# Kernel tuning notes

Measured on AMD Instinct MI355X. Metric: run time of the kernel, lower is better.

## Reference

```python
import jax, jax.numpy as jnp
import numpy as np

CHEB_K = 3


def setup_inputs() -> dict:
    key = jax.random.key(0)
    k1, k2, k3 = jax.random.split(key, 3)
    B, N, C = 64, 2048, 64
    E, O = 16, 64
    x = jax.random.normal(k1, (B, N, C), dtype=jnp.float32)
    node_embeddings = jax.random.normal(k2, (N, E), dtype=jnp.float32)
    # xavier-uniform-like init for weights_pool (embed_dim, cheb_k, dim_in, dim_out)
    fan_in, fan_out = E * CHEB_K * C, O
    limit = float(np.sqrt(6.0 / (fan_in + fan_out)))
    weights_pool = jax.random.uniform(k3, (E, CHEB_K, C, O), dtype=jnp.float32,
                                      minval=-limit, maxval=limit)
    bias_pool = jnp.zeros((E, O), dtype=jnp.float32)
    return {"x": x, "node_embeddings": node_embeddings,
            "weights_pool": weights_pool, "bias_pool": bias_pool}


def reference(x, node_embeddings, weights_pool, bias_pool):
    N = node_embeddings.shape[0]
    # adaptive adjacency: softmax(relu(E E^T)) row-wise   [N, N]
    supports = jax.nn.softmax(jax.nn.relu(node_embeddings @ node_embeddings.T), axis=1)
    # Chebyshev recurrence: T0 = I, T1 = A, Tk = 2*A*T_{k-1} - T_{k-2}
    support_set = [jnp.eye(N, dtype=supports.dtype), supports]
    for _ in range(2, CHEB_K):
        support_set.append(2.0 * supports @ support_set[-1] - support_set[-2])
    supports_k = jnp.stack(support_set, axis=0)  # [K, N, N]
    # per-node dynamic weights / bias from pools
    weights = jnp.einsum('nd,dkio->nkio', node_embeddings, weights_pool)  # [N,K,C,O]
    bias = node_embeddings @ bias_pool                                    # [N,O]
    # graph conv: gather Chebyshev features then per-node grouped GEMM
    x_g = jnp.einsum('knm,bmc->bnkc', supports_k, x)       # [B,N,K,C]
    x_gconv = jnp.einsum('bnki,nkio->bno', x_g, weights) + bias  # [B,N,O]
    return x_gconv
```

## Files before the change

### kernel.cpp

```cpp
#include <hip/hip_runtime.h>
#include <hip/hip_bf16.h>

#define BB 64
#define NN 2048
#define CC 64
#define EE 16
#define OO 64
#define JJ 4096

typedef __attribute__((ext_vector_type(8))) short short8;
typedef __attribute__((ext_vector_type(4))) float f32x4;
typedef __attribute__((ext_vector_type(4))) unsigned short u16x4;
typedef __attribute__((ext_vector_type(8))) unsigned short u16x8;

__device__ __forceinline__ unsigned short f2bf(float f) {
  __hip_bfloat16 h = __float2bfloat16(f);
  return *reinterpret_cast<unsigned short*>(&h);
}
__device__ __forceinline__ float bf2f(unsigned short u) {
  unsigned int v = ((unsigned int)u) << 16;
  return *reinterpret_cast<float*>(&v);
}
__device__ __forceinline__ void gload16(const void* g, void* l) {
  __builtin_amdgcn_global_load_lds(
      (const __attribute__((address_space(1))) unsigned int*)g,
      (__attribute__((address_space(3))) unsigned int*)l, 16, 0, 0);
}

__global__ __launch_bounds__(256) void supports_kernel(
    const float* __restrict__ emb, unsigned short* __restrict__ A)
{
  int n = blockIdx.x;
  int tid = threadIdx.x;
  float en[EE];
#pragma unroll
  for (int d = 0; d < EE; ++d) en[d] = emb[n*EE + d];

  float logit[8];
  float lmax = 0.0f;
#pragma unroll
  for (int i = 0; i < 8; ++i) {
    int m = i*256 + tid;
    const float* em = emb + m*EE;
    float s = 0.f;
#pragma unroll
    for (int d = 0; d < EE; ++d) s = fmaf(en[d], em[d], s);
    s = fmaxf(s, 0.f);
    logit[i] = s;
    lmax = fmaxf(lmax, s);
  }
  __shared__ float red[256];
  red[tid] = lmax; __syncthreads();
  for (int s = 128; s > 0; s >>= 1) {
    if (tid < s) red[tid] = fmaxf(red[tid], red[tid+s]);
    __syncthreads();
  }
  lmax = red[0]; __syncthreads();
  float sum = 0.f;
#pragma unroll
  for (int i = 0; i < 8; ++i) {
    float e = __expf(logit[i]-lmax);
    logit[i] = e; sum += e;
  }
  red[tid] = sum; __syncthreads();
  for (int s = 128; s > 0; s >>= 1) {
    if (tid < s) red[tid] += red[tid+s];
    __syncthreads();
  }
  float inv = 1.f/red[0];
#pragma unroll
  for (int i = 0; i < 8; ++i) A[(size_t)n*NN + i*256 + tid] = f2bf(logit[i]*inv);
}

__global__ __launch_bounds__(256) void xpose_kernel(
    const float* __restrict__ x, unsigned short* __restrict__ Xt)
{
  int b = blockIdx.y;
  int n0 = blockIdx.x * 64;
  __shared__ float T[64][65];
  int tid = threadIdx.x;
  int r = tid >> 4, c4 = (tid & 15) * 4;
  const float* src = x + ((size_t)b*NN + n0)*64;
#pragma unroll
  for (int rr = r; rr < 64; rr += 16) {
    float4 v = *(const float4*)(src + rr*64 + c4);
    T[rr][c4] = v.x; T[rr][c4+1] = v.y; T[rr][c4+2] = v.z; T[rr][c4+3] = v.w;
  }
  __syncthreads();
  int c = tid >> 2, q0 = (tid & 3) * 16;
  unsigned short* dst = Xt + ((size_t)b*64 + c)*NN + n0 + q0;
  u16x8 o0, o1;
#pragma unroll
  for (int q = 0; q < 8; ++q) o0[q] = f2bf(T[q0+q][c]);
#pragma unroll
  for (int q = 0; q < 8; ++q) o1[q] = f2bf(T[q0+8+q][c]);
  *(u16x8*)(dst) = o0;
  *(u16x8*)(dst + 8) = o1;
}

__global__ __launch_bounds__(256) void gemm_bt_bf16(
    const unsigned short* __restrict__ A, const unsigned short* __restrict__ Bt,
    unsigned short* __restrict__ Crow, unsigned short* __restrict__ Ct, int writeT)
{
  __shared__ unsigned short As[128*64];
  __shared__ unsigned short Bs[128*64];
  int tid = threadIdx.x;
  int bid = blockIdx.x;
  int swz = (bid & 7) * 64 + (bid >> 3);
  int m0 = (swz >> 5) * 128, j0 = (swz & 31) * 128;
  int wid = tid >> 6, lane = tid & 63;
  int wm = wid >> 1, wn = wid & 1;
  int fr = lane & 15, kg = lane >> 4;
  int lrow = lane >> 3, lu = lane & 7;

  f32x4 acc[4][4];
#pragma unroll
  for (int i = 0; i < 4; ++i)
#pragma unroll
    for (int j = 0; j < 4; ++j) acc[i][j] = (f32x4){0.f,0.f,0.f,0.f};

  for (int k0 = 0; k0 < 2048; k0 += 64) {
#pragma unroll
    for (int li = 0; li < 4; ++li) {
      int rb = wid*32 + li*8;
      int r = rb + lrow;
      int su = lu ^ (r & 7);
      gload16(A  + (size_t)(m0 + r)*2048 + k0 + su*8, &As[rb*64]);
      gload16(Bt + (size_t)(j0 + r)*2048 + k0 + su*8, &Bs[rb*64]);
    }
    asm volatile("s_waitcnt vmcnt(0)" ::: "memory");
    __syncthreads();
#pragma unroll
    for (int ks = 0; ks < 2; ++ks) {
      short8 af[4], bv[4];
#pragma unroll
      for (int i = 0; i < 4; ++i) {
        int r = wm*64 + i*16 + fr;
        int u = ((ks << 2) | kg) ^ (r & 7);
        af[i] = *(const short8*)((const char*)As + r*128 + u*16);
      }
#pragma unroll
      for (int j = 0; j < 4; ++j) {
        int r = wn*64 + j*16 + fr;
        int u = ((ks << 2) | kg) ^ (r & 7);
        bv[j] = *(const short8*)((const char*)Bs + r*128 + u*16);
      }
#pragma unroll
      for (int i = 0; i < 4; ++i)
#pragma unroll
        for (int j = 0; j < 4; ++j)
          acc[i][j] = __builtin_amdgcn_mfma_f32_16x16x32_bf16(af[i], bv[j], acc[i][j], 0, 0, 0);
    }
    __syncthreads();
  }
  int mrow4 = (lane >> 4) * 4;
#pragma unroll
  for (int i = 0; i < 4; ++i) {
    int mbase = m0 + wm*64 + i*16 + mrow4;
#pragma unroll
    for (int j = 0; j < 4; ++j) {
      int jcol = j0 + wn*64 + j*16 + fr;
      f32x4 v = acc[i][j];
      if (writeT) {
        u16x4 pk = { f2bf(v[0]), f2bf(v[1]), f2bf(v[2]), f2bf(v[3]) };
        *(u16x4*)(Ct + (size_t)jcol*2048 + mbase) = pk;
      }
      Crow[(size_t)(mbase+0)*4096 + jcol] = f2bf(v[0]);
      Crow[(size_t)(mbase+1)*4096 + jcol] = f2bf(v[1]);
      Crow[(size_t)(mbase+2)*4096 + jcol] = f2bf(v[2]);
      Crow[(size_t)(mbase+3)*4096 + jcol] = f2bf(v[3]);
    }
  }
}

__global__ __launch_bounds__(256) void wgen_kernel(
    const float* __restrict__ emb, const float* __restrict__ wp,
    unsigned short* __restrict__ wtg)
{
  __shared__ unsigned short Wlds[4][64*72];
  __shared__ float e_s[4][16];
  int tid = threadIdx.x;
  int g = blockIdx.x, r = blockIdx.y;
  int n0 = g*4;
  if (tid < 64) e_s[tid >> 4][tid & 15] = emb[n0*16 + tid];
  __syncthreads();
  int o = tid & 63, w = tid >> 6;
  float e0[16], e1[16], e2[16], e3[16];
#pragma unroll
  for (int d = 0; d < 16; ++d) {
    e0[d] = e_s[0][d]; e1[d] = e_s[1][d]; e2[d] = e_s[2][d]; e3[d] = e_s[3][d];
  }
#pragma unroll
  for (int p = 0; p < 2; ++p) {
    int u = r*8 + p*4 + w;
    float s0[8], s1[8], s2[8], s3[8];
#pragma unroll
    for (int q = 0; q < 8; ++q) { s0[q]=0.f; s1[q]=0.f; s2[q]=0.f; s3[q]=0.f; }
    const float* wpp = wp + u*512 + o;
#pragma unroll
    for (int d = 0; d < 16; ++d) {
#pragma unroll
      for (int q = 0; q < 8; ++q) {
        float wv = wpp[d*12288 + q*64];
        s0[q] = fmaf(e0[d], wv, s0[q]);
        s1[q] = fmaf(e1[d], wv, s1[q]);
        s2[q] = fmaf(e2[d], wv, s2[q]);
        s3[q] = fmaf(e3[d], wv, s3[q]);
      }
    }
    int slot = (u & 7) ^ (o & 7);
    u16x8 r0, r1, r2, r3;
#pragma unroll
    for (int q = 0; q < 8; ++q) {
      r0[q] = f2bf(s0[q]); r1[q] = f2bf(s1[q]);
      r2[q] = f2bf(s2[q]); r3[q] = f2bf(s3[q]);
    }
    *(u16x8*)&Wlds[0][o*72 + slot*8] = r0;
    *(u16x8*)&Wlds[1][o*72 + slot*8] = r1;
    *(u16x8*)&Wlds[2][o*72 + slot*8] = r2;
    *(u16x8*)&Wlds[3][o*72 + slot*8] = r3;
  }
  __syncthreads();
  int nd = tid >> 6;
  unsigned short* dst = wtg + (size_t)(n0+nd)*12288 + o*192 + r*64;
#pragma unroll
  for (int s = 0; s < 8; ++s)
    *(u16x8*)(dst + s*8) = *(const u16x8*)&Wlds[nd][o*72 + s*8];
}

#define FNPB 2
__global__ __launch_bounds__(256) void final_mfma(
    const float* __restrict__ x, const float* __restrict__ emb,
    const float* __restrict__ bp, const unsigned short* __restrict__ wtg,
    const unsigned short* __restrict__ y1, const unsigned short* __restrict__ y2,
    float* __restrict__ out)
{
  __shared__ unsigned short As[64*192];
  __shared__ unsigned short Ws[64*192];
  int tid = threadIdx.x;
  int lane = tid & 63, wid = tid >> 6;
  int b = tid & 63, quarter = tid >> 6;
  int fr = lane & 15, kg = lane >> 4;
  int o = wid*16 + fr;

  for (int inode = 0; inode < FNPB; ++inode) {
    int n = blockIdx.x * FNPB + inode;

#pragma unroll
    for (int i = 0; i < 6; ++i) {
      int base = wid*3072 + i*512;
      gload16(wtg + (size_t)n*12288 + base + lane*8, &Ws[base]);
    }

#pragma unroll
    for (int h = 0; h < 2; ++h) {
      int ul = quarter + h*4;
      const float* xp = x + ((size_t)b*NN + n)*64 + ul*8;
      float4 xv0 = *(const float4*)(xp);
      float4 xv1 = *(const float4*)(xp + 4);
      float fx[8] = {xv0.x,xv0.y,xv0.z,xv0.w,xv1.x,xv1.y,xv1.z,xv1.w};
      u16x8 v1 = *(const u16x8*)(y1 + (size_t)n*JJ + b*64 + ul*8);
      u16x8 v2 = *(const u16x8*)(y2 + (size_t)n*JJ + b*64 + ul*8);
      u16x8 xb, t2;
#pragma unroll
      for (int q = 0; q < 8; ++q) {
        xb[q] = f2bf(fx[q]);
        t2[q] = f2bf(2.f*bf2f(v2[q]) - fx[q]);
      }
      int sw = ul ^ (b & 7);
      *(u16x8*)&As[b*192 + sw*8]        = xb;
      *(u16x8*)&As[b*192 + (8|sw)*8]    = v1;
      *(u16x8*)&As[b*192 + (16|sw)*8]   = t2;
    }
    asm volatile("s_waitcnt vmcnt(0)" ::: "memory");
    __syncthreads();

    float breg = 0.f;
#pragma unroll
    for (int d = 0; d < 16; ++d) breg = fmaf(emb[n*16 + d], bp[d*64 + o], breg);
    f32x4 acc[4];
#pragma unroll
    for (int i = 0; i < 4; ++i) acc[i] = (f32x4){breg, breg, breg, breg};

#pragma unroll
    for (int ks = 0; ks < 6; ++ks) {
      int u = ks*4 + kg;
      int ro = wid*16 + fr;
      int ub = (u & ~7) | ((u & 7) ^ (ro & 7));
      short8 bv = *(const short8*)&Ws[ro*192 + ub*8];
#pragma unroll
      for (int i = 0; i < 4; ++i) {
        int ra = i*16 + fr;
        int ua = (u & ~7) | ((u & 7) ^ (ra & 7));
        short8 af = *(const short8*)&As[ra*192 + ua*8];
        acc[i] = __builtin_amdgcn_mfma_f32_16x16x32_bf16(af, bv, acc[i], 0, 0, 0);
      }
    }
    __syncthreads();

    int mrow = (lane >> 4) * 4;
#pragma unroll
    for (int i = 0; i < 4; ++i) {
#pragma unroll
      for (int r = 0; r < 4; ++r) {
        int brow = i*16 + mrow + r;
        out[((size_t)brow*NN + n)*64 + o] = acc[i][r];
      }
    }
  }
}

extern "C" void kernel_launch(void* const* d_in, const int* in_sizes, int n_in,
                              void* d_out, int out_size, void* d_ws, size_t ws_size,
                              hipStream_t stream) {
  const float* x   = (const float*)d_in[0];
  const float* emb = (const float*)d_in[1];
  const float* wp  = (const float*)d_in[2];
  const float* bp  = (const float*)d_in[3];
  float* out = (float*)d_out;

  unsigned short* Ab  = (unsigned short*)d_ws;
  unsigned short* Y1b = Ab  + (size_t)NN*NN;
  unsigned short* Y2b = Y1b + (size_t)NN*JJ;
  unsigned short* region = Y2b + (size_t)NN*JJ;
  unsigned short* Xt  = region;
  unsigned short* Y1T = region + (size_t)JJ*NN;
  unsigned short* Wtg = region;

  supports_kernel<<<NN, 256, 0, stream>>>(emb, Ab);
  xpose_kernel<<<dim3(32, 64), 256, 0, stream>>>(x, Xt);
  dim3 g(512);
  gemm_bt_bf16<<<g, 256, 0, stream>>>(Ab, Xt,  Y1b, Y1T, 1);
  gemm_bt_bf16<<<g, 256, 0, stream>>>(Ab, Y1T, Y2b, nullptr, 0);
  wgen_kernel<<<dim3(512, 3), 256, 0, stream>>>(emb, wp, Wtg);
  final_mfma<<<NN/FNPB, 256, 0, stream>>>(x, emb, bp, Wtg, Y1b, Y2b, out);
}
```

Measured before the change: 182.8 us.

## Double-buffer LDS tiles in bf16 GEMM to overlap global loads with MFMA

The GEMM kernel now keeps two LDS buffers for the A and B tiles. It issues the async global-to-LDS loads for the next K tile before computing on the current one, and waits only on the older loads with vmcnt(8). The intent is to hide global memory latency behind the matrix-core work instead of stalling each iteration on vmcnt(0). In exchange, LDS use doubles to 64KB per block, which may lower occupancy, and correctness now depends on the manual vmcnt and barrier ordering being right.

```diff
diff --git a/kernel.cpp b/kernel.cpp
--- a/kernel.cpp
+++ b/kernel.cpp
@@ -98,12 +98,27 @@
   *(u16x8*)(dst + 8) = o1;
 }
 
+__device__ __forceinline__ void stage_tile(
+    const unsigned short* __restrict__ A, const unsigned short* __restrict__ Bt,
+    unsigned short* as, unsigned short* bs,
+    int m0, int j0, int k0, int wid, int lrow, int lu)
+{
+#pragma unroll
+  for (int li = 0; li < 4; ++li) {
+    int rb = wid*32 + li*8;
+    int r = rb + lrow;
+    int su = lu ^ (r & 7);
+    gload16(A  + (size_t)(m0 + r)*2048 + k0 + su*8, as + rb*64);
+    gload16(Bt + (size_t)(j0 + r)*2048 + k0 + su*8, bs + rb*64);
+  }
+}
+
 __global__ __launch_bounds__(256) void gemm_bt_bf16(
     const unsigned short* __restrict__ A, const unsigned short* __restrict__ Bt,
     unsigned short* __restrict__ Crow, unsigned short* __restrict__ Ct, int writeT)
 {
-  __shared__ unsigned short As[128*64];
-  __shared__ unsigned short Bs[128*64];
+  __shared__ unsigned short As[2][128*64];
+  __shared__ unsigned short Bs[2][128*64];
   int tid = threadIdx.x;
   int bid = blockIdx.x;
   int swz = (bid & 7) * 64 + (bid >> 3);
@@ -119,17 +134,22 @@
 #pragma unroll
     for (int j = 0; j < 4; ++j) acc[i][j] = (f32x4){0.f,0.f,0.f,0.f};
 
+  stage_tile(A, Bt, As[0], Bs[0], m0, j0, 0, wid, lrow, lu);
+
+  int cur = 0;
+#pragma unroll 2
   for (int k0 = 0; k0 < 2048; k0 += 64) {
-#pragma unroll
-    for (int li = 0; li < 4; ++li) {
-      int rb = wid*32 + li*8;
-      int r = rb + lrow;
-      int su = lu ^ (r & 7);
-      gload16(A  + (size_t)(m0 + r)*2048 + k0 + su*8, &As[rb*64]);
-      gload16(Bt + (size_t)(j0 + r)*2048 + k0 + su*8, &Bs[rb*64]);
-    }
-    asm volatile("s_waitcnt vmcnt(0)" ::: "memory");
-    __syncthreads();
+    if (k0 + 64 < 2048) {
+      stage_tile(A, Bt, As[cur^1], Bs[cur^1], m0, j0, k0 + 64, wid, lrow, lu);
+      asm volatile("s_waitcnt vmcnt(8)" ::: "memory");
+    } else {
+      asm volatile("s_waitcnt vmcnt(0)" ::: "memory");
+    }
+    __builtin_amdgcn_s_barrier();
+    asm volatile("" ::: "memory");
+
+    const unsigned short* asb = As[cur];
+    const unsigned short* bsb = Bs[cur];
 #pragma unroll
     for (int ks = 0; ks < 2; ++ks) {
       short8 af[4], bv[4];
@@ -137,13 +157,13 @@
       for (int i = 0; i < 4; ++i) {
         int r = wm*64 + i*16 + fr;
         int u = ((ks << 2) | kg) ^ (r & 7);
-        af[i] = *(const short8*)((const char*)As + r*128 + u*16);
+        af[i] = *(const short8*)((const char*)asb + r*128 + u*16);
       }
 #pragma unroll
       for (int j = 0; j < 4; ++j) {
         int r = wn*64 + j*16 + fr;
         int u = ((ks << 2) | kg) ^ (r & 7);
-        bv[j] = *(const short8*)((const char*)Bs + r*128 + u*16);
+        bv[j] = *(const short8*)((const char*)bsb + r*128 + u*16);
       }
 #pragma unroll
       for (int i = 0; i < 4; ++i)
@@ -151,8 +171,11 @@
         for (int j = 0; j < 4; ++j)
           acc[i][j] = __builtin_amdgcn_mfma_f32_16x16x32_bf16(af[i], bv[j], acc[i][j], 0, 0, 0);
     }
-    __syncthreads();
-  }
+    asm volatile("" ::: "memory");
+    __builtin_amdgcn_s_barrier();
+    cur ^= 1;
+  }
+
   int mrow4 = (lane >> 4) * 4;
 #pragma unroll
   for (int i = 0; i < 4; ++i) {
```

Result: faster. 178.1 us (-2.6%).
